# Performance work log

Measured on AMD Instinct MI355X. Metric: run time of the kernel, lower is better.

The kernel has to match this reference:

```python
import jax, jax.numpy as jnp
import numpy as np

SEGMENTS = 64
SU2NDIM = 16
N = 16  # SU(2^4) matrix dimension
BATCH = 128


def setup_inputs() -> dict:
    key = jax.random.key(0)
    # Small scale keeps expm well-conditioned (skew-ish generators in practice)
    x = 0.1 * jax.random.normal(key, (BATCH, SEGMENTS * SU2NDIM, N, N), dtype=jnp.float32)
    return {"x": x}


def _batched_expm(a):
    # a: [..., N, N] -> expm over last two dims
    flat = a.reshape((-1, N, N))
    ex = jax.vmap(jax.scipy.linalg.expm)(flat)
    return ex.reshape(a.shape)


def reference(x):
    # maintensor = expm(-x), reversed along axis 0 (faithful to source)
    m = _batched_expm(-x)            # [B, S*D, N, N]
    m = m[::-1]                      # tf.reverse(maintensor, [0])
    b = m.shape[0]
    # tf.split along axis 1 into SEGMENTS contiguous chunks of SU2NDIM
    m = m.reshape(b, SEGMENTS, SU2NDIM, N, N)
    # Sequential chain product per segment: U = M[D-1] @ ... @ M[1] @ M[0] @ I
    ms = jnp.moveaxis(m, 2, 0)       # [D, B, S, N, N]
    u0 = jnp.broadcast_to(jnp.eye(N, dtype=x.dtype), (b, SEGMENTS, N, N))
    def step(u, mj):
        return mj @ u, None
    u, _ = jax.lax.scan(step, u0, ms)
    return u                         # [B, SEGMENTS, N, N] == transpose([1,0,2,3]) of stacked list
```

## Files before the change

kernel.cpp:

```cpp
#include <hip/hip_runtime.h>

typedef float f32x4 __attribute__((ext_vector_type(4)));
typedef short s16x8 __attribute__((ext_vector_type(8)));
typedef unsigned int uint;
typedef uint u32x4 __attribute__((ext_vector_type(4)));
typedef uint u32x2 __attribute__((ext_vector_type(2)));

union Frag {
  u32x4 u;
  s16x8 s;
};

__device__ __forceinline__ uint packhi(float f0, float f1) {
  uint a = __float_as_uint(f0) + 0x8000u;
  uint b = __float_as_uint(f1) + 0x8000u;
  return __builtin_amdgcn_perm(b, a, 0x07060302u);
}

__device__ __forceinline__ void split2(float f0, float f1, uint& hi, uint& lo) {
  uint a0 = __float_as_uint(f0) + 0x8000u;
  uint a1 = __float_as_uint(f1) + 0x8000u;
  hi = __builtin_amdgcn_perm(a1, a0, 0x07060302u);
  float h0 = __uint_as_float(a0 & 0xFFFF0000u);
  float h1 = __uint_as_float(a1 & 0xFFFF0000u);
  lo = packhi(f0 - h0, f1 - h1);
}

__device__ __forceinline__ u32x2 swap32(uint a, uint b) {
#if __has_builtin(__builtin_amdgcn_permlane32_swap)
  return __builtin_amdgcn_permlane32_swap(a, b, false, false);
#else
  __asm__("v_permlane32_swap_b32 %0, %1" : "+v"(a), "+v"(b));
  u32x2 r;
  r[0] = a;
  r[1] = b;
  return r;
#endif
}
__device__ __forceinline__ u32x2 swap16(uint a, uint b) {
#if __has_builtin(__builtin_amdgcn_permlane16_swap)
  return __builtin_amdgcn_permlane16_swap(a, b, false, false);
#else
  __asm__("v_permlane16_swap_b32 %0, %1" : "+v"(a), "+v"(b));
  u32x2 r;
  r[0] = a;
  r[1] = b;
  return r;
#endif
}

__device__ __forceinline__ u32x4 quadB(uint p, uint q) {
  u32x2 e = swap32(p, q);
  u32x2 f = swap16(e[0], e[1]);
  u32x2 r01 = swap32(f[0], f[0]);
  u32x2 r23 = swap32(f[1], f[1]);
  return (u32x4){r01[0], r01[1], r23[0], r23[1]};
}

__device__ __forceinline__ u32x4 quadA(uint h0, uint h1, uint l0, uint l1) {
  u32x2 e = swap32(h0, l0);
  u32x2 g = swap32(h1, l1);
  u32x2 a02 = swap16(e[0], e[1]);
  u32x2 a13 = swap16(g[0], g[1]);
  return (u32x4){a02[0], a13[0], a02[1], a13[1]};
}

__device__ __forceinline__ f32x4 expm_negT(const float* __restrict__ A, int lo,
                                           int g, int gt, bool low, f32x4 idm) {
  float c0 = A[(8 * gt + 0) * 16 + lo], c1 = A[(8 * gt + 1) * 16 + lo];
  float c2 = A[(8 * gt + 2) * 16 + lo], c3 = A[(8 * gt + 3) * 16 + lo];
  float c4 = A[(8 * gt + 4) * 16 + lo], c5 = A[(8 * gt + 5) * 16 + lo];
  float c6 = A[(8 * gt + 6) * 16 + lo], c7 = A[(8 * gt + 7) * 16 + lo];
  f32x4 xr = *(const f32x4*)(A + lo * 16 + 4 * g);
  uint h, lw;
  Frag xa;
  split2(c0, c1, h, lw);
  xa.u[0] = low ? h : lw;
  split2(c2, c3, h, lw);
  xa.u[1] = low ? h : lw;
  split2(c4, c5, h, lw);
  xa.u[2] = low ? h : lw;
  split2(c6, c7, h, lw);
  xa.u[3] = low ? h : lw;
  f32x4 t;
#pragma unroll
  for (int i = 0; i < 4; ++i)
    t[i] = fmaf(1.f / 720.f, xr[i], (-1.f / 120.f) * idm[i]);
  const float SK[5] = {1.f / 24.f, -1.f / 6.f, 0.5f, -1.f, 1.f};
#pragma unroll
  for (int k = 0; k < 5; ++k) {
    Frag tb;
    tb.u = quadB(packhi(t[0], t[1]), packhi(t[2], t[3]));
    f32x4 acc = idm * SK[k];
    t = __builtin_amdgcn_mfma_f32_16x16x32_bf16(xa.s, tb.s, acc, 0, 0, 0);
  }
  return t;
}

__global__ __launch_bounds__(256, 8) void unitary_kernel(
    const float* __restrict__ x, float* __restrict__ out) {
  const int tid = threadIdx.x;
  const int w = tid >> 6;
  const int l = tid & 63;
  const int lo = l & 15;
  const int g = l >> 4;
  const int gt = g & 1;
  const bool low = g < 2;

  const int ch = blockIdx.x * 4 + w;
  const float* xb =
      x + ((size_t)(127 - (ch >> 6)) * 1024 + (size_t)(ch & 63) * 16) * 256;

  f32x4 idm;
  idm[0] = (4 * g + 0 == lo) ? 1.f : 0.f;
  idm[1] = (4 * g + 1 == lo) ? 1.f : 0.f;
  idm[2] = (4 * g + 2 == lo) ? 1.f : 0.f;
  idm[3] = (4 * g + 3 == lo) ? 1.f : 0.f;

  Frag ifr;
  {
    uint v = ((lo >> 3) == gt) ? (0x3F80u << (16 * (lo & 1))) : 0u;
    int slot = (lo >> 1) & 3;
    ifr.u[0] = (slot == 0) ? v : 0u;
    ifr.u[1] = (slot == 1) ? v : 0u;
    ifr.u[2] = (slot == 2) ? v : 0u;
    ifr.u[3] = (slot == 3) ? v : 0u;
  }

  f32x4 uc;
#pragma unroll 1
  for (int j = 0; j < 16; ++j) {
    f32x4 et = expm_negT(xb + j * 256, lo, g, gt, low, idm);
    uint eh0, el0, eh1, el1;
    split2(et[0], et[1], eh0, el0);
    split2(et[2], et[3], eh1, el1);
    Frag ea;
    ea.u = quadA(eh0, eh1, el0, el1);
    f32x4 z = {0.f, 0.f, 0.f, 0.f};
    if (j) {
      uint uh0, ul0, uh1, ul1;
      split2(uc[0], uc[1], uh0, ul0);
      split2(uc[2], uc[3], uh1, ul1);
      Frag b1, b2;
      b1.u = quadB(uh0, uh1);
      b2.u = quadB(ul0, ul1);
      f32x4 t1 = __builtin_amdgcn_mfma_f32_16x16x32_bf16(ea.s, b1.s, z, 0, 0, 0);
      uc = __builtin_amdgcn_mfma_f32_16x16x32_bf16(ea.s, b2.s, t1, 0, 0, 0);
    } else {
      uc = __builtin_amdgcn_mfma_f32_16x16x32_bf16(ea.s, ifr.s, z, 0, 0, 0);
    }
  }

  float* op = out + (size_t)ch * 256;
  op[(4 * g + 0) * 16 + lo] = uc[0];
  op[(4 * g + 1) * 16 + lo] = uc[1];
  op[(4 * g + 2) * 16 + lo] = uc[2];
  op[(4 * g + 3) * 16 + lo] = uc[3];
}

extern "C" void kernel_launch(void* const* d_in, const int* in_sizes, int n_in,
                              void* d_out, int out_size, void* d_ws,
                              size_t ws_size, hipStream_t stream) {
  const float* x = (const float*)d_in[0];
  float* out = (float*)d_out;
  unitary_kernel<<<dim3(2048), dim3(256), 0, stream>>>(x, out);
}
```

Baseline: 194.0 us.

## Route chain-product operand shuffles through LDS and truncate bf16 splits

Measured after the change: 192.3 us. No clear change (-0.8%).

```diff
diff --git a/kernel.cpp b/kernel.cpp
--- a/kernel.cpp
+++ b/kernel.cpp
@@ -17,14 +17,18 @@
   return __builtin_amdgcn_perm(b, a, 0x07060302u);
 }
 
-__device__ __forceinline__ void split2(float f0, float f1, uint& hi, uint& lo) {
-  uint a0 = __float_as_uint(f0) + 0x8000u;
-  uint a1 = __float_as_uint(f1) + 0x8000u;
+__device__ __forceinline__ void splitT2(float f0, float f1, uint& hi,
+                                        uint& lo) {
+  uint a0 = __float_as_uint(f0);
+  uint a1 = __float_as_uint(f1);
   hi = __builtin_amdgcn_perm(a1, a0, 0x07060302u);
-  float h0 = __uint_as_float(a0 & 0xFFFF0000u);
-  float h1 = __uint_as_float(a1 & 0xFFFF0000u);
-  lo = packhi(f0 - h0, f1 - h1);
+  float r0 = f0 - __uint_as_float(a0 & 0xFFFF0000u);
+  float r1 = f1 - __uint_as_float(a1 & 0xFFFF0000u);
+  lo = __builtin_amdgcn_perm(__float_as_uint(r1), __float_as_uint(r0),
+                             0x07060302u);
 }
+
+#define CFENCE() __asm__ __volatile__("" ::: "memory")
 
 __device__ __forceinline__ u32x2 swap32(uint a, uint b) {
 #if __has_builtin(__builtin_amdgcn_permlane32_swap)
@@ -57,16 +61,9 @@
   return (u32x4){r01[0], r01[1], r23[0], r23[1]};
 }
 
-__device__ __forceinline__ u32x4 quadA(uint h0, uint h1, uint l0, uint l1) {
-  u32x2 e = swap32(h0, l0);
-  u32x2 g = swap32(h1, l1);
-  u32x2 a02 = swap16(e[0], e[1]);
-  u32x2 a13 = swap16(g[0], g[1]);
-  return (u32x4){a02[0], a13[0], a02[1], a13[1]};
-}
-
 __device__ __forceinline__ f32x4 expm_negT(const float* __restrict__ A, int lo,
-                                           int g, int gt, bool low, f32x4 idm) {
+                                           int g, int gt, bool low, f32x4 idm,
+                                           f32x4 idm120) {
   float c0 = A[(8 * gt + 0) * 16 + lo], c1 = A[(8 * gt + 1) * 16 + lo];
   float c2 = A[(8 * gt + 2) * 16 + lo], c3 = A[(8 * gt + 3) * 16 + lo];
   float c4 = A[(8 * gt + 4) * 16 + lo], c5 = A[(8 * gt + 5) * 16 + lo];
@@ -74,18 +71,17 @@
   f32x4 xr = *(const f32x4*)(A + lo * 16 + 4 * g);
   uint h, lw;
   Frag xa;
-  split2(c0, c1, h, lw);
+  splitT2(c0, c1, h, lw);
   xa.u[0] = low ? h : lw;
-  split2(c2, c3, h, lw);
+  splitT2(c2, c3, h, lw);
   xa.u[1] = low ? h : lw;
-  split2(c4, c5, h, lw);
+  splitT2(c4, c5, h, lw);
   xa.u[2] = low ? h : lw;
-  split2(c6, c7, h, lw);
+  splitT2(c6, c7, h, lw);
   xa.u[3] = low ? h : lw;
   f32x4 t;
 #pragma unroll
-  for (int i = 0; i < 4; ++i)
-    t[i] = fmaf(1.f / 720.f, xr[i], (-1.f / 120.f) * idm[i]);
+  for (int i = 0; i < 4; ++i) t[i] = fmaf(1.f / 720.f, xr[i], idm120[i]);
   const float SK[5] = {1.f / 24.f, -1.f / 6.f, 0.5f, -1.f, 1.f};
 #pragma unroll
   for (int k = 0; k < 5; ++k) {
@@ -99,6 +95,9 @@
 
 __global__ __launch_bounds__(256, 8) void unitary_kernel(
     const float* __restrict__ x, float* __restrict__ out) {
+  __shared__ uint PE[4][320];
+  __shared__ uint PU[4][320];
+
   const int tid = threadIdx.x;
   const int w = tid >> 6;
   const int l = tid & 63;
@@ -106,6 +105,9 @@
   const int g = l >> 4;
   const int gt = g & 1;
   const bool low = g < 2;
+
+  uint* pe = PE[w];
+  uint* pu = PU[w];
 
   const int ch = blockIdx.x * 4 + w;
   const float* xb =
@@ -116,6 +118,7 @@
   idm[1] = (4 * g + 1 == lo) ? 1.f : 0.f;
   idm[2] = (4 * g + 2 == lo) ? 1.f : 0.f;
   idm[3] = (4 * g + 3 == lo) ? 1.f : 0.f;
+  f32x4 idm120 = idm * (-1.f / 120.f);
 
   Frag ifr;
   {
@@ -127,26 +130,47 @@
     ifr.u[3] = (slot == 3) ? v : 0u;
   }
 
+  uint* pew = pe + lo * 20 + 4 * g;
+  const uint* pea = pe + lo * 20 + 8 * gt + (low ? 0 : 2);
+  uint* puw = pu + lo * 20 + 4 * g;
+  const uint* pub = pu + lo * 20 + 8 * gt;
+
   f32x4 uc;
 #pragma unroll 1
   for (int j = 0; j < 16; ++j) {
-    f32x4 et = expm_negT(xb + j * 256, lo, g, gt, low, idm);
-    uint eh0, el0, eh1, el1;
-    split2(et[0], et[1], eh0, el0);
-    split2(et[2], et[3], eh1, el1);
+    f32x4 et = expm_negT(xb + j * 256, lo, g, gt, low, idm, idm120);
+    uint h0, l0, h1, l1;
+    splitT2(et[0], et[1], h0, l0);
+    splitT2(et[2], et[3], h1, l1);
+    *(u32x4*)pew = (u32x4){h0, h1, l0, l1};
+    if (j) {
+      splitT2(uc[0], uc[1], h0, l0);
+      splitT2(uc[2], uc[3], h1, l1);
+      *(u32x4*)puw = (u32x4){h0, h1, l0, l1};
+    }
+    CFENCE();
     Frag ea;
-    ea.u = quadA(eh0, eh1, el0, el1);
+    ea.u[0] = pea[0];
+    ea.u[1] = pea[1];
+    ea.u[2] = pea[4];
+    ea.u[3] = pea[5];
     f32x4 z = {0.f, 0.f, 0.f, 0.f};
     if (j) {
-      uint uh0, ul0, uh1, ul1;
-      split2(uc[0], uc[1], uh0, ul0);
-      split2(uc[2], uc[3], uh1, ul1);
       Frag b1, b2;
-      b1.u = quadB(uh0, uh1);
-      b2.u = quadB(ul0, ul1);
-      f32x4 t1 = __builtin_amdgcn_mfma_f32_16x16x32_bf16(ea.s, b1.s, z, 0, 0, 0);
+      b1.u[0] = pub[0];
+      b1.u[1] = pub[1];
+      b1.u[2] = pub[4];
+      b1.u[3] = pub[5];
+      b2.u[0] = pub[2];
+      b2.u[1] = pub[3];
+      b2.u[2] = pub[6];
+      b2.u[3] = pub[7];
+      CFENCE();
+      f32x4 t1 =
+          __builtin_amdgcn_mfma_f32_16x16x32_bf16(ea.s, b1.s, z, 0, 0, 0);
       uc = __builtin_amdgcn_mfma_f32_16x16x32_bf16(ea.s, b2.s, t1, 0, 0, 0);
     } else {
+      CFENCE();
       uc = __builtin_amdgcn_mfma_f32_16x16x32_bf16(ea.s, ifr.s, z, 0, 0, 0);
     }
   }
```
